# Kernel optimization log

Hardware: AMD Instinct MI355X
Metric: run time of the kernel (lower is better)

## Reference

```python
import jax, jax.numpy as jnp
import numpy as np

EPS = 1e-5
D_MODEL = 1024
NUM_HEADS = 16
D_HEAD = D_MODEL // NUM_HEADS


def _exp_map(v, c):
    # (1/sqrt(c)) * tanh(sqrt(c)*||v||) * v/||v||
    sqrt_c = jnp.sqrt(c)
    n = jnp.maximum(jnp.linalg.norm(v, axis=-1, keepdims=True), EPS)
    return jnp.tanh(sqrt_c * n) / (sqrt_c * n) * v


def _log_map(y, c):
    sqrt_c = jnp.sqrt(c)
    n = jnp.maximum(jnp.linalg.norm(y, axis=-1, keepdims=True), EPS)
    n_cl = jnp.minimum(n, 1.0 / sqrt_c - EPS)
    return jnp.arctanh(sqrt_c * n_cl) / (sqrt_c * n) * y


def _poincare_distance(x, y, c):
    # x, y: (B, H, N, d). Returns (B, H, N, N).
    xns = jnp.sum(x * x, axis=-1, keepdims=True)          # (B,H,N,1)
    yns = jnp.sum(y * y, axis=-1, keepdims=True)          # (B,H,N,1)
    dot = jnp.einsum('bhnd,bhmd->bhnm', x, y)             # (B,H,N,N)
    yns_t = jnp.swapaxes(yns, -1, -2)                     # (B,H,1,N)
    diff_sq = xns - 2.0 * dot + yns_t
    denom = (1.0 - c * xns) * (1.0 - c * yns_t)
    arg = 1.0 + 2.0 * c * diff_sq / jnp.maximum(denom, EPS)
    return jnp.arccosh(jnp.maximum(arg, 1.0 + EPS)) / jnp.sqrt(c)


def setup_inputs() -> dict:
    key = jax.random.key(0)
    ks = jax.random.split(key, 6)
    B, N = 1, 2048
    x = jax.random.normal(ks[0], (B, N, D_MODEL), dtype=jnp.float32)
    s = 0.02
    W_q = jax.random.normal(ks[1], (D_MODEL, D_MODEL), dtype=jnp.float32) * s
    W_k = jax.random.normal(ks[2], (D_MODEL, D_MODEL), dtype=jnp.float32) * s
    W_v = jax.random.normal(ks[3], (D_MODEL, D_MODEL), dtype=jnp.float32) * s
    W_o = jax.random.normal(ks[4], (D_MODEL, D_MODEL), dtype=jnp.float32) * s
    mask = jnp.tril(jnp.ones((N, N), dtype=bool))[None, None]  # (1,1,N,N) causal
    return {
        'x': x, 'W_q': W_q, 'W_k': W_k, 'W_v': W_v, 'W_o': W_o,
        'log_c': jnp.float32(0.0), 'beta': jnp.float32(0.0),
        'attention_bias': jnp.float32(0.0), 'mask': mask,
    }


def reference(x, W_q, W_k, W_v, W_o, log_c, beta, attention_bias, mask):
    B, N, _ = x.shape
    c = jax.nn.softplus(log_c)
    # nn.Linear(bias=False): y = x @ W.T
    q_t = (x @ W_q.T).reshape(B, N, NUM_HEADS, D_HEAD).transpose(0, 2, 1, 3)
    k_t = (x @ W_k.T).reshape(B, N, NUM_HEADS, D_HEAD).transpose(0, 2, 1, 3)
    v_t = (x @ W_v.T).reshape(B, N, NUM_HEADS, D_HEAD).transpose(0, 2, 1, 3)
    # map q, k onto the Poincare ball
    q = _exp_map(q_t, c)
    k = _exp_map(k_t, c)
    dist = _poincare_distance(q, k, c)                    # (B,H,N,N)
    beta_pos = jax.nn.softplus(beta)
    scores = -beta_pos * dist - attention_bias
    neg_big = -jnp.finfo(jnp.float32).max
    scores = jnp.where(mask, scores, neg_big)
    weights = jax.nn.softmax(scores, axis=-1)
    out_tangent = jnp.einsum('bhnm,bhmd->bhnd', weights, v_t)
    out_hyper = _exp_map(out_tangent, c)
    out_tangent_heads = _log_map(out_hyper, c)
    concat = out_tangent_heads.transpose(0, 2, 1, 3).reshape(B, N, D_MODEL)
    return concat @ W_o.T
```

## Files before the change

kernel.cpp:

```cpp
#include <hip/hip_runtime.h>
#include <stdint.h>

#define EPSF 1e-5f

typedef float f32x4 __attribute__((ext_vector_type(4)));
typedef short bf16x8 __attribute__((ext_vector_type(8)));

__device__ __forceinline__ float softplus_f(float x) {
    return x > 20.f ? x : log1pf(expf(x));
}

__device__ __forceinline__ unsigned short f2bf(float f) {
    union { float f; unsigned int u; } v; v.f = f;
    unsigned int r = v.u + 0x7FFFu + ((v.u >> 16) & 1u);
    return (unsigned short)(r >> 16);
}
__device__ __forceinline__ float bf2f(unsigned short u) {
    union { unsigned int i; float f; } v; v.i = ((unsigned int)u) << 16;
    return v.f;
}
__device__ __forceinline__ int cvt_pk_bf16(float a, float b) {
    int d;
    asm("v_cvt_pk_bf16_f32 %0, %1, %2" : "=v"(d) : "v"(a), "v"(b));
    return d;
}
__device__ __forceinline__ int bperm(int byte_addr, int v) {
    return __builtin_amdgcn_ds_bpermute(byte_addr, v);
}
__device__ __forceinline__ float bpermf(int byte_addr, float v) {
    return __int_as_float(__builtin_amdgcn_ds_bpermute(byte_addr, __float_as_int(v)));
}
__device__ __forceinline__ float rcp_f(float x)  { float d; asm("v_rcp_f32 %0, %1"  : "=v"(d) : "v"(x)); return d; }
__device__ __forceinline__ float sqrt_f(float x) { float d; asm("v_sqrt_f32 %0, %1" : "=v"(d) : "v"(x)); return d; }
__device__ __forceinline__ float log2_f(float x) { float d; asm("v_log_f32 %0, %1"  : "=v"(d) : "v"(x)); return d; }
__device__ __forceinline__ float exp2_f(float x) { float d; asm("v_exp_f32 %0, %1"  : "=v"(d) : "v"(x)); return d; }

__global__ __launch_bounds__(256) void k_f2b_all(const float* __restrict__ x,
                                                 const float* __restrict__ W0, const float* __restrict__ W1,
                                                 const float* __restrict__ W2, const float* __restrict__ W3,
                                                 unsigned short* __restrict__ xb,
                                                 unsigned short* __restrict__ o0, unsigned short* __restrict__ o1,
                                                 unsigned short* __restrict__ o2, unsigned short* __restrict__ o3) {
    const int NX4 = 524288;
    const int NW4 = 262144;
    int i = blockIdx.x * 256 + threadIdx.x;
    int stride = gridDim.x * 256;
    for (; i < NX4 + 4 * NW4; i += stride) {
        const float4* src;
        ushort4* dst;
        if (i < NX4) {
            src = (const float4*)x + i;
            dst = (ushort4*)xb + i;
        } else {
            int j = i - NX4;
            int sel = j >> 18, off = j & (NW4 - 1);
            const float* s = sel == 0 ? W0 : sel == 1 ? W1 : sel == 2 ? W2 : W3;
            unsigned short* d = sel == 0 ? o0 : sel == 1 ? o1 : sel == 2 ? o2 : o3;
            src = (const float4*)s + off;
            dst = (ushort4*)d + off;
        }
        float4 v = *src;
        ushort4 o;
        o.x = f2bf(v.x); o.y = f2bf(v.y); o.z = f2bf(v.z); o.w = f2bf(v.w);
        *dst = o;
    }
}

#if defined(__has_builtin)
#if __has_builtin(__builtin_amdgcn_global_load_lds)
#define HAVE_GLL 1
#endif
#endif

template <int QKV>
__global__ __launch_bounds__(256) void k_gemm128(const unsigned short* __restrict__ A,
                                                 const unsigned short* __restrict__ B,
                                                 void* __restrict__ C0, void* __restrict__ C1,
                                                 void* __restrict__ C2,
                                                 int M, int N, int K) {
    __shared__ __align__(16) unsigned short As[128 * 32];
    __shared__ __align__(16) unsigned short Bs[128 * 32];
    const int tid  = threadIdx.x;
    const int lane = tid & 63;
    const int w    = tid >> 6;
    const int wr   = w >> 1, wc = w & 1;
    const int fr   = lane & 15;
    const int fg   = lane >> 4;
    const int nbx  = N >> 7;
    const int bx   = blockIdx.x % nbx;
    const int by   = blockIdx.x / nbx;
    const int bm0  = by * 128, bn0 = bx * 128;

    const int lrow = lane >> 2;
    const int lcol = (lane & 3) * 8;

    f32x4 acc[4][4] = {};

    for (int kk = 0; kk < K; kk += 32) {
#ifdef HAVE_GLL
        {
            const unsigned short* ga0 = &A[(size_t)(bm0 + w * 16 + lrow) * K + kk + lcol];
            __builtin_amdgcn_global_load_lds((const __attribute__((address_space(1))) void*)ga0,
                (__attribute__((address_space(3))) void*)&As[(w * 16) * 32], 16, 0, 0);
            const unsigned short* ga1 = &A[(size_t)(bm0 + 64 + w * 16 + lrow) * K + kk + lcol];
            __builtin_amdgcn_global_load_lds((const __attribute__((address_space(1))) void*)ga1,
                (__attribute__((address_space(3))) void*)&As[(64 + w * 16) * 32], 16, 0, 0);
            const unsigned short* gb0 = &B[(size_t)(bn0 + w * 16 + lrow) * K + kk + lcol];
            __builtin_amdgcn_global_load_lds((const __attribute__((address_space(1))) void*)gb0,
                (__attribute__((address_space(3))) void*)&Bs[(w * 16) * 32], 16, 0, 0);
            const unsigned short* gb1 = &B[(size_t)(bn0 + 64 + w * 16 + lrow) * K + kk + lcol];
            __builtin_amdgcn_global_load_lds((const __attribute__((address_space(1))) void*)gb1,
                (__attribute__((address_space(3))) void*)&Bs[(64 + w * 16) * 32], 16, 0, 0);
        }
#else
        {
            uint4 a0 = *(const uint4*)&A[(size_t)(bm0 + w * 16 + lrow) * K + kk + lcol];
            uint4 a1 = *(const uint4*)&A[(size_t)(bm0 + 64 + w * 16 + lrow) * K + kk + lcol];
            uint4 b0 = *(const uint4*)&B[(size_t)(bn0 + w * 16 + lrow) * K + kk + lcol];
            uint4 b1 = *(const uint4*)&B[(size_t)(bn0 + 64 + w * 16 + lrow) * K + kk + lcol];
            *(uint4*)&As[(w * 16 + lrow) * 32 + lcol]      = a0;
            *(uint4*)&As[(64 + w * 16 + lrow) * 32 + lcol] = a1;
            *(uint4*)&Bs[(w * 16 + lrow) * 32 + lcol]      = b0;
            *(uint4*)&Bs[(64 + w * 16 + lrow) * 32 + lcol] = b1;
        }
#endif
        __syncthreads();

        bf16x8 av[4], bv[4];
#pragma unroll
        for (int m = 0; m < 4; m++)
            av[m] = *(const bf16x8*)&As[(wr * 64 + m * 16 + fr) * 32 + fg * 8];
#pragma unroll
        for (int n = 0; n < 4; n++)
            bv[n] = *(const bf16x8*)&Bs[(wc * 64 + n * 16 + fr) * 32 + fg * 8];
#pragma unroll
        for (int m = 0; m < 4; m++)
#pragma unroll
            for (int n = 0; n < 4; n++)
                acc[m][n] = __builtin_amdgcn_mfma_f32_16x16x32_bf16(av[m], bv[n], acc[m][n], 0, 0, 0);
        __syncthreads();
    }

    const int crow0 = bm0 + wr * 64 + fg * 4;
    if (QKV) {
        const int sel = bn0 >> 10;
        const int lc0 = (bn0 & 1023) + wc * 64 + fr;
        unsigned short* Cp = (unsigned short*)(sel == 0 ? C0 : sel == 1 ? C1 : C2);
#pragma unroll
        for (int m = 0; m < 4; m++)
#pragma unroll
            for (int n = 0; n < 4; n++)
#pragma unroll
                for (int r = 0; r < 4; r++)
                    Cp[(size_t)(crow0 + m * 16 + r) * 1024 + lc0 + n * 16] =
                        f2bf(acc[m][n][r]);
    } else {
        float* Cf = (float*)C0;
        const int ccol0 = bn0 + wc * 64 + fr;
#pragma unroll
        for (int m = 0; m < 4; m++)
#pragma unroll
            for (int n = 0; n < 4; n++)
#pragma unroll
                for (int r = 0; r < 4; r++)
                    Cf[(size_t)(crow0 + m * 16 + r) * N + ccol0 + n * 16] =
                        acc[m][n][r];
    }
}

template <int QKV>
__global__ __launch_bounds__(256) void k_gemm_gll(const unsigned short* __restrict__ A,
                                                  const unsigned short* __restrict__ B,
                                                  void* __restrict__ C0, void* __restrict__ C1,
                                                  void* __restrict__ C2,
                                                  int M, int N, int K) {
    __shared__ __align__(16) unsigned short As[128 * 32];
    __shared__ __align__(16) unsigned short Bs[64 * 32];
    const int tid  = threadIdx.x;
    const int lane = tid & 63;
    const int w    = tid >> 6;
    const int wr   = w >> 1, wc = w & 1;
    const int fr   = lane & 15;
    const int fg   = lane >> 4;
    const int nbx  = N >> 6;
    const int bx   = blockIdx.x % nbx;
    const int by   = blockIdx.x / nbx;
    const int bm0  = by * 128, bn0 = bx * 64;

    const int lrow = lane >> 2;
    const int lcol = (lane & 3) * 8;

    f32x4 acc[4][2] = {};

    for (int kk = 0; kk < K; kk += 32) {
#ifdef HAVE_GLL
        {
            const unsigned short* gp0 = &A[(size_t)(bm0 + w * 16 + lrow) * K + kk + lcol];
            __builtin_amdgcn_global_load_lds((const __attribute__((address_space(1))) void*)gp0,
                (__attribute__((address_space(3))) void*)&As[(w * 16) * 32], 16, 0, 0);
            const unsigned short* gp1 = &A[(size_t)(bm0 + 64 + w * 16 + lrow) * K + kk + lcol];
            __builtin_amdgcn_global_load_lds((const __attribute__((address_space(1))) void*)gp1,
                (__attribute__((address_space(3))) void*)&As[(64 + w * 16) * 32], 16, 0, 0);
            const unsigned short* gp2 = &B[(size_t)(bn0 + w * 16 + lrow) * K + kk + lcol];
            __builtin_amdgcn_global_load_lds((const __attribute__((address_space(1))) void*)gp2,
                (__attribute__((address_space(3))) void*)&Bs[(w * 16) * 32], 16, 0, 0);
        }
#else
        {
            uint4 a0 = *(const uint4*)&A[(size_t)(bm0 + w * 16 + lrow) * K + kk + lcol];
            uint4 a1 = *(const uint4*)&A[(size_t)(bm0 + 64 + w * 16 + lrow) * K + kk + lcol];
            uint4 b0 = *(const uint4*)&B[(size_t)(bn0 + w * 16 + lrow) * K + kk + lcol];
            *(uint4*)&As[(w * 16 + lrow) * 32 + lcol]      = a0;
            *(uint4*)&As[(64 + w * 16 + lrow) * 32 + lcol] = a1;
            *(uint4*)&Bs[(w * 16 + lrow) * 32 + lcol]      = b0;
        }
#endif
        __syncthreads();

        bf16x8 av[4], bv[2];
#pragma unroll
        for (int m = 0; m < 4; m++)
            av[m] = *(const bf16x8*)&As[(wr * 64 + m * 16 + fr) * 32 + fg * 8];
#pragma unroll
        for (int n = 0; n < 2; n++)
            bv[n] = *(const bf16x8*)&Bs[(wc * 32 + n * 16 + fr) * 32 + fg * 8];
#pragma unroll
        for (int m = 0; m < 4; m++)
#pragma unroll
            for (int n = 0; n < 2; n++)
                acc[m][n] = __builtin_amdgcn_mfma_f32_16x16x32_bf16(av[m], bv[n], acc[m][n], 0, 0, 0);
        __syncthreads();
    }

    const int crow0 = bm0 + wr * 64 + fg * 4;
    if (QKV) {
        const int sel = bn0 >> 10;
        const int lc0 = bn0 & 1023;
        unsigned short* Cp = (unsigned short*)(sel == 0 ? C0 : sel == 1 ? C1 : C2);
#pragma unroll
        for (int m = 0; m < 4; m++)
#pragma unroll
            for (int n = 0; n < 2; n++)
#pragma unroll
                for (int r = 0; r < 4; r++)
                    Cp[(size_t)(crow0 + m * 16 + r) * 1024 + lc0 + wc * 32 + n * 16 + fr] =
                        f2bf(acc[m][n][r]);
    } else {
        float* Cf = (float*)C0;
#pragma unroll
        for (int m = 0; m < 4; m++)
#pragma unroll
            for (int n = 0; n < 2; n++)
#pragma unroll
                for (int r = 0; r < 4; r++)
                    Cf[(size_t)(crow0 + m * 16 + r) * N + bn0 + wc * 32 + n * 16 + fr] =
                        acc[m][n][r];
    }
}

__global__ __launch_bounds__(256) void k_vt(const unsigned short* __restrict__ Vb,
                                            unsigned short* __restrict__ Vtg) {
    __shared__ unsigned short T[64][72];
    const int b = blockIdx.x;
    const int h = b & 15;
    const int n0 = (b >> 4) << 6;
    const int tid = threadIdx.x;
#pragma unroll
    for (int p = 0; p < 2; p++) {
        int idx = tid + p * 256;
        int r = idx >> 3, cbv = (idx & 7) * 8;
        *(uint4*)&T[r][cbv] = *(const uint4*)&Vb[(size_t)(n0 + r) * 1024 + h * 64 + cbv];
    }
    __syncthreads();
#pragma unroll
    for (int p = 0; p < 2; p++) {
        int idx = tid + p * 256;
        int d = idx >> 3, nb = (idx & 7) * 8;
        bf16x8 tv;
#pragma unroll
        for (int j = 0; j < 8; j++) tv[j] = (short)T[nb + j][d];
        *(bf16x8*)&Vtg[(size_t)(h * 64 + d) * 2048 + n0 + nb] = tv;
    }
}

__global__ __launch_bounds__(256) void k_expmap2(unsigned short* __restrict__ Qb,
                                                 unsigned short* __restrict__ Kb,
                                                 float* __restrict__ xns, float* __restrict__ xds,
                                                 float* __restrict__ yns, float* __restrict__ yds,
                                                 const float* __restrict__ pLogC) {
    float c  = softplus_f(pLogC[0]);
    float sc = sqrtf(c);
    const int bid = blockIdx.x;
    const bool isK = bid >= 8192;
    unsigned short* QK = isK ? Kb : Qb;
    float* ns = isK ? yns : xns;
    float* ds = isK ? yds : xds;
    int gid  = ((bid & 8191) * 256 + threadIdx.x) >> 6;
    int lane = threadIdx.x & 63;
    int n = gid >> 4, h = gid & 15;
    size_t idx = (size_t)n * 1024 + h * 64 + lane;
    float v  = bf2f(QK[idx]);
    float n2 = v * v;
#pragma unroll
    for (int o = 1; o < 64; o <<= 1) n2 += __shfl_xor(n2, o);
    float nn = fmaxf(sqrtf(n2), EPSF);
    float u  = sc * nn;
    float e  = __expf(-2.f * u);
    float th = (1.f - e) / (1.f + e);
    float f  = th / (sc * nn);
    QK[idx]  = f2bf(f * v);
    if (lane == 0) {
        float xn = f * f * n2;
        ns[h * 2048 + n] = xn;
        float op = 1.f + e;
        float sech2 = 4.f * e / (op * op);
        ds[h * 2048 + n] = (n2 < 1e-6f) ? (1.f - c * xn) : sech2;
    }
}

__global__ __launch_bounds__(256) void k_attn_part(const unsigned short* __restrict__ Qb,
                                                   const unsigned short* __restrict__ Kb,
                                                   const unsigned short* __restrict__ Vtg,
                                                   const float* __restrict__ xns,
                                                   const float* __restrict__ xds,
                                                   const float* __restrict__ yns,
                                                   const float* __restrict__ yds,
                                                   const float* __restrict__ pLogC,
                                                   const float* __restrict__ pBeta,
                                                   unsigned short* __restrict__ Og,
                                                   float* __restrict__ ml,
                                                   unsigned short* __restrict__ conc) {
    __shared__ __align__(16) unsigned short Ks[64][72];
    __shared__ __align__(16) unsigned short Vt[64][72];
    __shared__ __align__(16) float yl[64];
    __shared__ __align__(16) float ydl[64];

    const float c      = softplus_f(pLogC[0]);
    const float sc     = sqrtf(c);
    const float inv_sc = 1.f / sc;
    const float bpos   = softplus_f(pBeta[0]);
    const float b2     = bpos * inv_sc;
    const float twoc   = 2.f * c;
    const float m4c    = -4.f * c;

    const int b = 2303 - blockIdx.x;
    const int h = b / 144;
    const int t = b % 144;
    const int a = (t >= 4) + (t >= 12) + (t >= 24) + (t >= 40) + (t >= 60) + (t >= 84) + (t >= 112);
    const int r0_ = t - 2 * a * (a + 1);
    const int nch = a + 1;
    const int qt  = 4 * a + r0_ / nch;
    const int ci  = r0_ - (r0_ / nch) * nch;
    const int jt0 = ci * (qt + 1) / nch;
    const int jt1 = (ci + 1) * (qt + 1) / nch;
    const int q0  = qt << 6;
    const int slot = b;
    const bool full = (a == 0);

    const int tid  = threadIdx.x;
    const int lane = tid & 63;
    const int w    = tid >> 6;
    const int wq0  = w * 16;
    const int fr   = lane & 15;
    const int fg   = lane >> 4;
    const int rS   = tid >> 3;
    const int cS   = (tid & 7) * 8;

    const int qglob = q0 + wq0 + fr;
    const float xi2 = twoc * xns[h * 2048 + qglob];
    const float dxr = xds[h * 2048 + qglob];

    const unsigned short* qp = &Qb[(size_t)qglob * 1024 + h * 64 + fg * 8];
    const bf16x8 qb0 = *(const bf16x8*)qp;
    const bf16x8 qb1 = *(const bf16x8*)(qp + 32);

    float lrow = 0.f;
    f32x4 acc[4] = {};

    uint4 kr0, kr1, vr0, vr1;
    float ylr = 0.f;
#define LOAD_TILE(jtv) do { int kb = (jtv) << 6; \
    kr0 = *(const uint4*)&Kb[(size_t)(kb + rS) * 1024 + h * 64 + cS]; \
    kr1 = *(const uint4*)&Kb[(size_t)(kb + 32 + rS) * 1024 + h * 64 + cS]; \
    vr0 = *(const uint4*)&Vtg[(size_t)(h * 64 + rS) * 2048 + kb + cS]; \
    vr1 = *(const uint4*)&Vtg[(size_t)(h * 64 + 32 + rS) * 2048 + kb + cS]; \
    if (tid < 64) ylr = yns[h * 2048 + kb + tid]; \
    else if (tid < 128) ylr = yds[h * 2048 + kb + tid - 64]; \
} while (0)

#define XFORM(DOMASK) do { \
    _Pragma("unroll") for (int tn = 0; tn < 4; tn++) { \
        float4 yv  = *(const float4*)&yl[tn * 16 + fg * 4];    \
        float4 ydv = *(const float4*)&ydl[tn * 16 + fg * 4]; \
        _Pragma("unroll") for (int r = 0; r < 4; r++) { \
            float diff2 = fmaf(st[tn][r], m4c, xi2 + (&yv.x)[r]); \
            float den   = fmaxf(dxr * (&ydv.x)[r], EPSF); \
            float tt    = fmaxf(diff2 * rcp_f(den), EPSF); \
            float wv    = 1.f + tt + sqrt_f(tt * (tt + 2.f)); \
            float sv    = -b2 * log2_f(wv); \
            if (DOMASK && (k0 + tn * 16 + fg * 4 + r > qglob)) sv = -3.0e38f; \
            p[tn][r] = exp2_f(sv);            \
        } \
    } \
} while (0)

    LOAD_TILE(jt0);
    for (int jt = jt0; jt < jt1; ++jt) {
        const int k0 = jt << 6;
        __syncthreads();
        *(uint4*)&Ks[rS][cS]      = kr0;
        *(uint4*)&Ks[32 + rS][cS] = kr1;
        *(uint4*)&Vt[rS][cS]      = vr0;
        *(uint4*)&Vt[32 + rS][cS] = vr1;
        if (tid < 64)       yl[tid]       = twoc * ylr;
        else if (tid < 128) ydl[tid - 64] = ylr;
        __syncthreads();
        if (jt + 1 < jt1) LOAD_TILE(jt + 1);

        f32x4 st[4] = {};
#pragma unroll
        for (int tn = 0; tn < 4; tn++) {
            bf16x8 ka0 = *(const bf16x8*)&Ks[tn * 16 + fr][fg * 8];
            bf16x8 ka1 = *(const bf16x8*)&Ks[tn * 16 + fr][32 + fg * 8];
            st[tn] = __builtin_amdgcn_mfma_f32_16x16x32_bf16(ka0, qb0, st[tn], 0, 0, 0);
            st[tn] = __builtin_amdgcn_mfma_f32_16x16x32_bf16(ka1, qb1, st[tn], 0, 0, 0);
        }

        float p[4][4];
        if (jt == qt) XFORM(1); else XFORM(0);

        {
            float r0 = (p[0][0] + p[0][1]) + (p[0][2] + p[0][3]);
            float r1 = (p[1][0] + p[1][1]) + (p[1][2] + p[1][3]);
            float r2 = (p[2][0] + p[2][1]) + (p[2][2] + p[2][3]);
            float r3 = (p[3][0] + p[3][1]) + (p[3][2] + p[3][3]);
            lrow += (r0 + r1) + (r2 + r3);
        }

        int lo[4], hi[4];
#pragma unroll
        for (int tn = 0; tn < 4; tn++) {
            lo[tn] = cvt_pk_bf16(p[tn][0], p[tn][1]);
            hi[tn] = cvt_pk_bf16(p[tn][2], p[tn][3]);
        }
        const int adrA = (fr + ((fg & 1) << 5)) << 2;
        const int adrB = adrA + 64;
        const bool hiSel = (fg >= 2);
        union PU { int i[4]; bf16x8 v; };
        PU pu0, pu1;
#pragma unroll
        for (int kh = 0; kh < 2; kh++) {
            int l0 = bperm(adrA, lo[2 * kh]);
            int l1 = bperm(adrA, lo[2 * kh + 1]);
            int h0 = bperm(adrA, hi[2 * kh]);
            int h1 = bperm(adrA, hi[2 * kh + 1]);
            int l0b = bperm(adrB, lo[2 * kh]);
            int l1b = bperm(adrB, lo[2 * kh + 1]);
            int h0b = bperm(adrB, hi[2 * kh]);
            int h1b = bperm(adrB, hi[2 * kh + 1]);
            PU& pu = kh ? pu1 : pu0;
            pu.i[0] = hiSel ? l1 : l0;
            pu.i[1] = hiSel ? h1 : h0;
            pu.i[2] = hiSel ? l1b : l0b;
            pu.i[3] = hiSel ? h1b : h0b;
        }
        bf16x8 pa0 = pu0.v, pa1 = pu1.v;

#pragma unroll
        for (int tn = 0; tn < 4; tn++) {
            bf16x8 vb0 = *(const bf16x8*)&Vt[tn * 16 + fr][fg * 8];
            bf16x8 vb1 = *(const bf16x8*)&Vt[tn * 16 + fr][32 + fg * 8];
            acc[tn] = __builtin_amdgcn_mfma_f32_16x16x32_bf16(pa0, vb0, acc[tn], 0, 0, 0);
            acc[tn] = __builtin_amdgcn_mfma_f32_16x16x32_bf16(pa1, vb1, acc[tn], 0, 0, 0);
        }
    }
#undef LOAD_TILE
#undef XFORM

    lrow += __shfl_xor(lrow, 16);
    lrow += __shfl_xor(lrow, 32);

    if (full) {
        float lr[4];
#pragma unroll
        for (int r = 0; r < 4; r++) lr[r] = bpermf((fg * 4 + r) << 2, lrow);
#pragma unroll
        for (int r = 0; r < 4; r++) {
            float rl = 1.f / lr[r];
            float tvv[4];
            float n2 = 0.f;
#pragma unroll
            for (int tn = 0; tn < 4; tn++) { tvv[tn] = acc[tn][r] * rl; n2 += tvv[tn] * tvv[tn]; }
#pragma unroll
            for (int o = 1; o < 16; o <<= 1) n2 += __shfl_xor(n2, o);
            float nt   = fmaxf(sqrtf(n2), EPSF);
            float f1   = tanhf(sc * nt) / (sc * nt);
            float ny   = fmaxf(f1 * sqrtf(n2), EPSF);
            float ncl  = fminf(ny, inv_sc - EPSF);
            float coef = atanhf(sc * ncl) / (sc * ny);
            int row = q0 + wq0 + fg * 4 + r;
#pragma unroll
            for (int tn = 0; tn < 4; tn++)
                conc[(size_t)row * 1024 + h * 64 + tn * 16 + fr] = f2bf(coef * f1 * tvv[tn]);
        }
    } else {
        if (fg == 0)
            ml[(size_t)slot * 64 + wq0 + fr] = lrow;
#pragma unroll
        for (int r = 0; r < 4; r++) {
            int row = wq0 + fg * 4 + r;
#pragma unroll
            for (int tn = 0; tn < 4; tn++)
                Og[(size_t)slot * 4096 + row * 64 + tn * 16 + fr] = f2bf(acc[tn][r]);
        }
    }
}

__global__ __launch_bounds__(256) void k_merge(const unsigned short* __restrict__ Og,
                                               const float* __restrict__ ml,
                                               const float* __restrict__ pLogC,
                                               unsigned short* __restrict__ conc) {
    const float c      = softplus_f(pLogC[0]);
    const float sc     = sqrtf(c);
    const float inv_sc = 1.f / sc;
    int gid2 = (blockIdx.x * 256 + threadIdx.x) >> 6;
    int lane = threadIdx.x & 63;
    int h = gid2 / 1792;
    int i = 256 + (gid2 - h * 1792);
    int qt = i >> 6, row = i & 63;
    int a = qt >> 2;
    int nch = a + 1;
    int slot0 = h * 144 + 2 * a * (a + 1) + (qt & 3) * (a + 1);

    float L = 0.f, O = 0.f;
    for (int k = 0; k < nch; k++) {
        L += ml[(size_t)(slot0 + k) * 64 + row];
        O += bf2f(Og[(size_t)(slot0 + k) * 4096 + row * 64 + lane]);
    }
    float tv = O / L;
    float n2 = tv * tv;
#pragma unroll
    for (int o = 1; o < 64; o <<= 1) n2 += __shfl_xor(n2, o);
    float nt   = fmaxf(sqrtf(n2), EPSF);
    float f1   = tanhf(sc * nt) / (sc * nt);
    float ny   = fmaxf(f1 * sqrtf(n2), EPSF);
    float ncl  = fminf(ny, inv_sc - EPSF);
    float coef = atanhf(sc * ncl) / (sc * ny);
    conc[(size_t)i * 1024 + h * 64 + lane] = f2bf(coef * f1 * tv);
}

extern "C" void kernel_launch(void* const* d_in, const int* in_sizes, int n_in,
                              void* d_out, int out_size, void* d_ws, size_t ws_size,
                              hipStream_t stream) {
    const float* x     = (const float*)d_in[0];
    const float* Wq    = (const float*)d_in[1];
    const float* Wk    = (const float*)d_in[2];
    const float* Wv    = (const float*)d_in[3];
    const float* Wo    = (const float*)d_in[4];
    const float* pLogC = (const float*)d_in[5];
    const float* pBeta = (const float*)d_in[6];
    float* out = (float*)d_out;

    char* w = (char*)d_ws;
    unsigned short* Vtg   = (unsigned short*)(w);
    unsigned short* Qtb   = (unsigned short*)(w + (4u  << 20));
    unsigned short* Ktb   = (unsigned short*)(w + (8u  << 20));
    unsigned short* concb = (unsigned short*)(w + (12u << 20));
    float*          xns   = (float*)(w + (16u << 20));
    float*          yns   = (float*)(w + (16u << 20) + (1u << 17));
    float*          xds   = (float*)(w + (16u << 20) + (2u << 17));
    float*          yds   = (float*)(w + (16u << 20) + (3u << 17));
    unsigned short* wob   = (unsigned short*)(w + (16u << 20) + (1u << 19));
    unsigned short* xb    = (unsigned short*)(w + (18u << 20) + (1u << 19));
    unsigned short* wqb   = (unsigned short*)(w + (22u << 20) + (1u << 19));
    unsigned short* wkb   = (unsigned short*)(w + (24u << 20) + (1u << 19));
    unsigned short* wvb   = (unsigned short*)(w + (26u << 20) + (1u << 19));
    unsigned short* Vb    = (unsigned short*)(w + (28u << 20) + (1u << 19));
    unsigned short* Og    = (unsigned short*)(w + (18u << 20) + (1u << 19));
    float*          ml    = (float*)(w + (36u << 20) + (1u << 19));

    k_f2b_all<<<2048, 256, 0, stream>>>(x, Wq, Wk, Wv, Wo, xb, wqb, wkb, wvb, wob);

    k_gemm128<1><<<384, 256, 0, stream>>>(xb, wqb, Qtb, Ktb, Vb, 2048, 3072, 1024);

    k_vt<<<512, 256, 0, stream>>>(Vb, Vtg);

    k_expmap2<<<16384, 256, 0, stream>>>(Qtb, Ktb, xns, xds, yns, yds, pLogC);

    k_attn_part<<<2304, 256, 0, stream>>>(Qtb, Ktb, Vtg, xns, xds, yns, yds,
                                          pLogC, pBeta, Og, ml, concb);

    k_merge<<<7168, 256, 0, stream>>>(Og, ml, pLogC, concb);

    k_gemm_gll<0><<<256, 256, 0, stream>>>(concb, wob, out, nullptr, nullptr,
                                           2048, 1024, 1024);
}
```

Measured before the change: 149.6 us.

## Split-K output GEMM, smaller QKV tiles, fuse V-transpose with expmap

Replaces the 128x128 QKV GEMM with the 128x64 tile kernel at 768 blocks so more CUs get work. Fuses the V transpose and the exp-map kernels into a single launch. Makes the output projection a 2-way split-K GEMM (512 blocks) that accumulates with float atomics into an output zeroed by a memset. This adds atomic traffic, an extra memset, and nondeterministic summation order.

After: 151.5 us. About the same (+1.3%).

```diff
diff --git a/kernel.cpp b/kernel.cpp
--- a/kernel.cpp
+++ b/kernel.cpp
@@ -73,102 +73,6 @@
 #endif
 
 template <int QKV>
-__global__ __launch_bounds__(256) void k_gemm128(const unsigned short* __restrict__ A,
-                                                 const unsigned short* __restrict__ B,
-                                                 void* __restrict__ C0, void* __restrict__ C1,
-                                                 void* __restrict__ C2,
-                                                 int M, int N, int K) {
-    __shared__ __align__(16) unsigned short As[128 * 32];
-    __shared__ __align__(16) unsigned short Bs[128 * 32];
-    const int tid  = threadIdx.x;
-    const int lane = tid & 63;
-    const int w    = tid >> 6;
-    const int wr   = w >> 1, wc = w & 1;
-    const int fr   = lane & 15;
-    const int fg   = lane >> 4;
-    const int nbx  = N >> 7;
-    const int bx   = blockIdx.x % nbx;
-    const int by   = blockIdx.x / nbx;
-    const int bm0  = by * 128, bn0 = bx * 128;
-
-    const int lrow = lane >> 2;
-    const int lcol = (lane & 3) * 8;
-
-    f32x4 acc[4][4] = {};
-
-    for (int kk = 0; kk < K; kk += 32) {
-#ifdef HAVE_GLL
-        {
-            const unsigned short* ga0 = &A[(size_t)(bm0 + w * 16 + lrow) * K + kk + lcol];
-            __builtin_amdgcn_global_load_lds((const __attribute__((address_space(1))) void*)ga0,
-                (__attribute__((address_space(3))) void*)&As[(w * 16) * 32], 16, 0, 0);
-            const unsigned short* ga1 = &A[(size_t)(bm0 + 64 + w * 16 + lrow) * K + kk + lcol];
-            __builtin_amdgcn_global_load_lds((const __attribute__((address_space(1))) void*)ga1,
-                (__attribute__((address_space(3))) void*)&As[(64 + w * 16) * 32], 16, 0, 0);
-            const unsigned short* gb0 = &B[(size_t)(bn0 + w * 16 + lrow) * K + kk + lcol];
-            __builtin_amdgcn_global_load_lds((const __attribute__((address_space(1))) void*)gb0,
-                (__attribute__((address_space(3))) void*)&Bs[(w * 16) * 32], 16, 0, 0);
-            const unsigned short* gb1 = &B[(size_t)(bn0 + 64 + w * 16 + lrow) * K + kk + lcol];
-            __builtin_amdgcn_global_load_lds((const __attribute__((address_space(1))) void*)gb1,
-                (__attribute__((address_space(3))) void*)&Bs[(64 + w * 16) * 32], 16, 0, 0);
-        }
-#else
-        {
-            uint4 a0 = *(const uint4*)&A[(size_t)(bm0 + w * 16 + lrow) * K + kk + lcol];
-            uint4 a1 = *(const uint4*)&A[(size_t)(bm0 + 64 + w * 16 + lrow) * K + kk + lcol];
-            uint4 b0 = *(const uint4*)&B[(size_t)(bn0 + w * 16 + lrow) * K + kk + lcol];
-            uint4 b1 = *(const uint4*)&B[(size_t)(bn0 + 64 + w * 16 + lrow) * K + kk + lcol];
-            *(uint4*)&As[(w * 16 + lrow) * 32 + lcol]      = a0;
-            *(uint4*)&As[(64 + w * 16 + lrow) * 32 + lcol] = a1;
-            *(uint4*)&Bs[(w * 16 + lrow) * 32 + lcol]      = b0;
-            *(uint4*)&Bs[(64 + w * 16 + lrow) * 32 + lcol] = b1;
-        }
-#endif
-        __syncthreads();
-
-        bf16x8 av[4], bv[4];
-#pragma unroll
-        for (int m = 0; m < 4; m++)
-            av[m] = *(const bf16x8*)&As[(wr * 64 + m * 16 + fr) * 32 + fg * 8];
-#pragma unroll
-        for (int n = 0; n < 4; n++)
-            bv[n] = *(const bf16x8*)&Bs[(wc * 64 + n * 16 + fr) * 32 + fg * 8];
-#pragma unroll
-        for (int m = 0; m < 4; m++)
-#pragma unroll
-            for (int n = 0; n < 4; n++)
-                acc[m][n] = __builtin_amdgcn_mfma_f32_16x16x32_bf16(av[m], bv[n], acc[m][n], 0, 0, 0);
-        __syncthreads();
-    }
-
-    const int crow0 = bm0 + wr * 64 + fg * 4;
-    if (QKV) {
-        const int sel = bn0 >> 10;
-        const int lc0 = (bn0 & 1023) + wc * 64 + fr;
-        unsigned short* Cp = (unsigned short*)(sel == 0 ? C0 : sel == 1 ? C1 : C2);
-#pragma unroll
-        for (int m = 0; m < 4; m++)
-#pragma unroll
-            for (int n = 0; n < 4; n++)
-#pragma unroll
-                for (int r = 0; r < 4; r++)
-                    Cp[(size_t)(crow0 + m * 16 + r) * 1024 + lc0 + n * 16] =
-                        f2bf(acc[m][n][r]);
-    } else {
-        float* Cf = (float*)C0;
-        const int ccol0 = bn0 + wc * 64 + fr;
-#pragma unroll
-        for (int m = 0; m < 4; m++)
-#pragma unroll
-            for (int n = 0; n < 4; n++)
-#pragma unroll
-                for (int r = 0; r < 4; r++)
-                    Cf[(size_t)(crow0 + m * 16 + r) * N + ccol0 + n * 16] =
-                        acc[m][n][r];
-    }
-}
-
-template <int QKV>
 __global__ __launch_bounds__(256) void k_gemm_gll(const unsigned short* __restrict__ A,
                                                   const unsigned short* __restrict__ B,
                                                   void* __restrict__ C0, void* __restrict__ C1,
@@ -258,63 +162,140 @@
     }
 }
 
-__global__ __launch_bounds__(256) void k_vt(const unsigned short* __restrict__ Vb,
-                                            unsigned short* __restrict__ Vtg) {
+__global__ __launch_bounds__(256) void k_gemm_sk(const unsigned short* __restrict__ A,
+                                                 const unsigned short* __restrict__ B,
+                                                 float* __restrict__ C,
+                                                 int M, int N, int K) {
+    __shared__ __align__(16) unsigned short As[128 * 32];
+    __shared__ __align__(16) unsigned short Bs[64 * 32];
+    const int tid  = threadIdx.x;
+    const int lane = tid & 63;
+    const int w    = tid >> 6;
+    const int wr   = w >> 1, wc = w & 1;
+    const int fr   = lane & 15;
+    const int fg   = lane >> 4;
+    const int nbx  = N >> 6;
+    const int half = blockIdx.x >> 8;
+    const int rem  = blockIdx.x & 255;
+    const int bx   = rem % nbx;
+    const int by   = rem / nbx;
+    const int bm0  = by * 128, bn0 = bx * 64;
+    const int kbeg = half * 512, kend = kbeg + 512;
+
+    const int lrow = lane >> 2;
+    const int lcol = (lane & 3) * 8;
+
+    f32x4 acc[4][2] = {};
+
+    for (int kk = kbeg; kk < kend; kk += 32) {
+#ifdef HAVE_GLL
+        {
+            const unsigned short* gp0 = &A[(size_t)(bm0 + w * 16 + lrow) * K + kk + lcol];
+            __builtin_amdgcn_global_load_lds((const __attribute__((address_space(1))) void*)gp0,
+                (__attribute__((address_space(3))) void*)&As[(w * 16) * 32], 16, 0, 0);
+            const unsigned short* gp1 = &A[(size_t)(bm0 + 64 + w * 16 + lrow) * K + kk + lcol];
+            __builtin_amdgcn_global_load_lds((const __attribute__((address_space(1))) void*)gp1,
+                (__attribute__((address_space(3))) void*)&As[(64 + w * 16) * 32], 16, 0, 0);
+            const unsigned short* gp2 = &B[(size_t)(bn0 + w * 16 + lrow) * K + kk + lcol];
+            __builtin_amdgcn_global_load_lds((const __attribute__((address_space(1))) void*)gp2,
+                (__attribute__((address_space(3))) void*)&Bs[(w * 16) * 32], 16, 0, 0);
+        }
+#else
+        {
+            uint4 a0 = *(const uint4*)&A[(size_t)(bm0 + w * 16 + lrow) * K + kk + lcol];
+            uint4 a1 = *(const uint4*)&A[(size_t)(bm0 + 64 + w * 16 + lrow) * K + kk + lcol];
+            uint4 b0 = *(const uint4*)&B[(size_t)(bn0 + w * 16 + lrow) * K + kk + lcol];
+            *(uint4*)&As[(w * 16 + lrow) * 32 + lcol]      = a0;
+            *(uint4*)&As[(64 + w * 16 + lrow) * 32 + lcol] = a1;
+            *(uint4*)&Bs[(w * 16 + lrow) * 32 + lcol]      = b0;
+        }
+#endif
+        __syncthreads();
+
+        bf16x8 av[4], bv[2];
+#pragma unroll
+        for (int m = 0; m < 4; m++)
+            av[m] = *(const bf16x8*)&As[(wr * 64 + m * 16 + fr) * 32 + fg * 8];
+#pragma unroll
+        for (int n = 0; n < 2; n++)
+            bv[n] = *(const bf16x8*)&Bs[(wc * 32 + n * 16 + fr) * 32 + fg * 8];
+#pragma unroll
+        for (int m = 0; m < 4; m++)
+#pragma unroll
+            for (int n = 0; n < 2; n++)
+                acc[m][n] = __builtin_amdgcn_mfma_f32_16x16x32_bf16(av[m], bv[n], acc[m][n], 0, 0, 0);
+        __syncthreads();
+    }
+
+    const int crow0 = bm0 + wr * 64 + fg * 4;
+#pragma unroll
+    for (int m = 0; m < 4; m++)
+#pragma unroll
+        for (int n = 0; n < 2; n++)
+#pragma unroll
+            for (int r = 0; r < 4; r++)
+                atomicAdd(&C[(size_t)(crow0 + m * 16 + r) * N + bn0 + wc * 32 + n * 16 + fr],
+                          acc[m][n][r]);
+}
+
+__global__ __launch_bounds__(256) void k_vt_expmap(const unsigned short* __restrict__ Vb,
+                                                   unsigned short* __restrict__ Vtg,
+                                                   unsigned short* __restrict__ Qb,
+                                                   unsigned short* __restrict__ Kb,
+                                                   float* __restrict__ xns, float* __restrict__ xds,
+                                                   float* __restrict__ yns, float* __restrict__ yds,
+                                                   const float* __restrict__ pLogC) {
     __shared__ unsigned short T[64][72];
-    const int b = blockIdx.x;
-    const int h = b & 15;
-    const int n0 = (b >> 4) << 6;
-    const int tid = threadIdx.x;
-#pragma unroll
-    for (int p = 0; p < 2; p++) {
-        int idx = tid + p * 256;
-        int r = idx >> 3, cbv = (idx & 7) * 8;
-        *(uint4*)&T[r][cbv] = *(const uint4*)&Vb[(size_t)(n0 + r) * 1024 + h * 64 + cbv];
-    }
-    __syncthreads();
-#pragma unroll
-    for (int p = 0; p < 2; p++) {
-        int idx = tid + p * 256;
-        int d = idx >> 3, nb = (idx & 7) * 8;
-        bf16x8 tv;
-#pragma unroll
-        for (int j = 0; j < 8; j++) tv[j] = (short)T[nb + j][d];
-        *(bf16x8*)&Vtg[(size_t)(h * 64 + d) * 2048 + n0 + nb] = tv;
-    }
-}
-
-__global__ __launch_bounds__(256) void k_expmap2(unsigned short* __restrict__ Qb,
-                                                 unsigned short* __restrict__ Kb,
-                                                 float* __restrict__ xns, float* __restrict__ xds,
-                                                 float* __restrict__ yns, float* __restrict__ yds,
-                                                 const float* __restrict__ pLogC) {
-    float c  = softplus_f(pLogC[0]);
-    float sc = sqrtf(c);
-    const int bid = blockIdx.x;
-    const bool isK = bid >= 8192;
-    unsigned short* QK = isK ? Kb : Qb;
-    float* ns = isK ? yns : xns;
-    float* ds = isK ? yds : xds;
-    int gid  = ((bid & 8191) * 256 + threadIdx.x) >> 6;
-    int lane = threadIdx.x & 63;
-    int n = gid >> 4, h = gid & 15;
-    size_t idx = (size_t)n * 1024 + h * 64 + lane;
-    float v  = bf2f(QK[idx]);
-    float n2 = v * v;
-#pragma unroll
-    for (int o = 1; o < 64; o <<= 1) n2 += __shfl_xor(n2, o);
-    float nn = fmaxf(sqrtf(n2), EPSF);
-    float u  = sc * nn;
-    float e  = __expf(-2.f * u);
-    float th = (1.f - e) / (1.f + e);
-    float f  = th / (sc * nn);
-    QK[idx]  = f2bf(f * v);
-    if (lane == 0) {
-        float xn = f * f * n2;
-        ns[h * 2048 + n] = xn;
-        float op = 1.f + e;
-        float sech2 = 4.f * e / (op * op);
-        ds[h * 2048 + n] = (n2 < 1e-6f) ? (1.f - c * xn) : sech2;
+    if (blockIdx.x < 512) {
+        const int b = blockIdx.x;
+        const int h = b & 15;
+        const int n0 = (b >> 4) << 6;
+        const int tid = threadIdx.x;
+#pragma unroll
+        for (int p = 0; p < 2; p++) {
+            int idx = tid + p * 256;
+            int r = idx >> 3, cbv = (idx & 7) * 8;
+            *(uint4*)&T[r][cbv] = *(const uint4*)&Vb[(size_t)(n0 + r) * 1024 + h * 64 + cbv];
+        }
+        __syncthreads();
+#pragma unroll
+        for (int p = 0; p < 2; p++) {
+            int idx = tid + p * 256;
+            int d = idx >> 3, nb = (idx & 7) * 8;
+            bf16x8 tv;
+#pragma unroll
+            for (int j = 0; j < 8; j++) tv[j] = (short)T[nb + j][d];
+            *(bf16x8*)&Vtg[(size_t)(h * 64 + d) * 2048 + n0 + nb] = tv;
+        }
+    } else {
+        float c  = softplus_f(pLogC[0]);
+        float sc = sqrtf(c);
+        const int bid = blockIdx.x - 512;
+        const bool isK = bid >= 8192;
+        unsigned short* QK = isK ? Kb : Qb;
+        float* ns = isK ? yns : xns;
+        float* ds = isK ? yds : xds;
+        int gid  = ((bid & 8191) * 256 + threadIdx.x) >> 6;
+        int lane = threadIdx.x & 63;
+        int n = gid >> 4, h = gid & 15;
+        size_t idx = (size_t)n * 1024 + h * 64 + lane;
+        float v  = bf2f(QK[idx]);
+        float n2 = v * v;
+#pragma unroll
+        for (int o = 1; o < 64; o <<= 1) n2 += __shfl_xor(n2, o);
+        float nn = fmaxf(sqrtf(n2), EPSF);
+        float u  = sc * nn;
+        float e  = __expf(-2.f * u);
+        float th = (1.f - e) / (1.f + e);
+        float f  = th / (sc * nn);
+        QK[idx]  = f2bf(f * v);
+        if (lane == 0) {
+            float xn = f * f * n2;
+            ns[h * 2048 + n] = xn;
+            float op = 1.f + e;
+            float sech2 = 4.f * e / (op * op);
+            ds[h * 2048 + n] = (n2 < 1e-6f) ? (1.f - c * xn) : sech2;
+        }
     }
 }
 
@@ -579,19 +560,19 @@
     unsigned short* Og    = (unsigned short*)(w + (18u << 20) + (1u << 19));
     float*          ml    = (float*)(w + (36u << 20) + (1u << 19));
 
+    hipMemsetAsync(out, 0, (size_t)2048 * 1024 * sizeof(float), stream);
+
     k_f2b_all<<<2048, 256, 0, stream>>>(x, Wq, Wk, Wv, Wo, xb, wqb, wkb, wvb, wob);
 
-    k_gemm128<1><<<384, 256, 0, stream>>>(xb, wqb, Qtb, Ktb, Vb, 2048, 3072, 1024);
-
-    k_vt<<<512, 256, 0, stream>>>(Vb, Vtg);
-
-    k_expmap2<<<16384, 256, 0, stream>>>(Qtb, Ktb, xns, xds, yns, yds, pLogC);
+    k_gemm_gll<1><<<768, 256, 0, stream>>>(xb, wqb, Qtb, Ktb, Vb, 2048, 3072, 1024);
+
+    k_vt_expmap<<<16896, 256, 0, stream>>>(Vb, Vtg, Qtb, Ktb,
+                                           xns, xds, yns, yds, pLogC);
 
     k_attn_part<<<2304, 256, 0, stream>>>(Qtb, Ktb, Vtg, xns, xds, yns, yds,
                                           pLogC, pBeta, Og, ml, concb);
 
     k_merge<<<7168, 256, 0, stream>>>(Og, ml, pLogC, concb);
 
-    k_gemm_gll<0><<<256, 256, 0, stream>>>(concb, wob, out, nullptr, nullptr,
-                                           2048, 1024, 1024);
-}
+    k_gemm_sk<<<512, 256, 0, stream>>>(concb, wob, out, 2048, 1024, 1024);
+}
```
